# Kernel tuning notes

Measured on AMD Instinct MI355X. Metric: run time of the kernel, lower is better.

## Reference

```python
import jax, jax.numpy as jnp
import numpy as np

EPSILON = 0.1      # init kwarg epsilon
NUM_STAB = 1e-06   # init kwarg num_stab
B, D, C = 4096, 3072, 10


def setup_inputs() -> dict:
    key = jax.random.key(0)
    k1, k2 = jax.random.split(key)
    data = jax.random.normal(k1, (B, D), dtype=jnp.float32)
    # small scale keeps softmax probs near-uniform -> rho well-conditioned
    W = jax.random.normal(k2, (D, C), dtype=jnp.float32) * 0.02
    return {"data": data, "W": W}


def _probs(logits, c):
    # output = softmax(...) * (1 - c*num_stab) + num_stab  (numerical stabilization)
    p = jax.nn.softmax(logits, axis=-1)
    return p * (1.0 - c * NUM_STAB) + NUM_STAB


def reference(data, W):
    c = W.shape[1]
    m = c - 1

    def g(x):  # x: [D] -> new_output row: [m]
        p = _probs(x @ W, c)
        s = jnp.sqrt(p)
        return 2.0 * s[:m] / (1.0 - s[m])

    # Vectorized Jacobian: replaces the m sequential autograd.grad calls.
    jac = jax.vmap(jax.jacrev(g))(data)            # [B, m, D]

    p = _probs(data @ W, c)                        # [B, C]
    s_m = jnp.sqrt(p[:, m])                        # [B]
    delta = 2.0 * jnp.arccos(jnp.sqrt(p / c).sum(axis=1))   # [B]
    rho = (2.0 * (1.0 - s_m) - p[:, :m].sum(axis=1)) / (1.0 - s_m)  # [B]
    jac_norm = jnp.sqrt(jnp.square(jac).sum(axis=(1, 2)))   # [B] Frobenius norm per sample
    reg = jax.nn.elu(jac_norm - delta / (rho * EPSILON))
    return reg.mean()
```

## Files before the change

kernel.cpp:

```cpp
#include <hip/hip_runtime.h>
#include <math.h>

#define NB 4096
#define ND 3072
#define NC 10
#define NM 9

static constexpr float kEps     = 0.1f;
static constexpr float kNumStab = 1e-6f;
static constexpr float kAlpha   = 1.0f - (float)NC * kNumStab;
static constexpr float kInvSqrtC = 0.31622776601683794f;

__global__ void gram_kernel(const float* __restrict__ W, float* __restrict__ G) {
    const int j = blockIdx.x / NC;
    const int k = blockIdx.x % NC;
    float acc = 0.0f;
    for (int d = threadIdx.x; d < ND; d += 256) {
        acc += W[d * NC + j] * W[d * NC + k];
    }
    #pragma unroll
    for (int off = 32; off > 0; off >>= 1) acc += __shfl_xor(acc, off, 64);
    __shared__ float part[4];
    const int lane = threadIdx.x & 63;
    const int wv   = threadIdx.x >> 6;
    if (lane == 0) part[wv] = acc;
    __syncthreads();
    if (threadIdx.x == 0) G[blockIdx.x] = part[0] + part[1] + part[2] + part[3];
}

__global__ __launch_bounds__(256) void jacreg_kernel(
        const float* __restrict__ data, const float* __restrict__ W,
        const float* __restrict__ G, float* __restrict__ out) {
    __shared__ float Gs[100];
    __shared__ float zpart[4][40];
    __shared__ float zsum[40];
    __shared__ float regs[4];

    const int tid  = threadIdx.x;
    const int lane = tid & 63;
    const int wv   = tid >> 6;
    if (tid < 100) Gs[tid] = G[tid];

    const int s0 = blockIdx.x * 4;

    float acc[4][10];
    #pragma unroll
    for (int s = 0; s < 4; ++s)
        #pragma unroll
        for (int k = 0; k < NC; ++k) acc[s][k] = 0.0f;

    const int dwave = wv * 768;
    #pragma unroll
    for (int it = 0; it < 3; ++it) {
        const int d0 = dwave + it * 256 + lane * 4;
        float4 xv[4];
        #pragma unroll
        for (int s = 0; s < 4; ++s) {
            xv[s] = *reinterpret_cast<const float4*>(
                        &data[(size_t)(s0 + s) * ND + d0]);
        }
        #pragma unroll
        for (int dd = 0; dd < 4; ++dd) {
            const float* wr = &W[(size_t)(d0 + dd) * NC];
            const float2 w01 = *reinterpret_cast<const float2*>(wr);
            const float2 w23 = *reinterpret_cast<const float2*>(wr + 2);
            const float2 w45 = *reinterpret_cast<const float2*>(wr + 4);
            const float2 w67 = *reinterpret_cast<const float2*>(wr + 6);
            const float2 w89 = *reinterpret_cast<const float2*>(wr + 8);
            const float wk[10] = {w01.x, w01.y, w23.x, w23.y, w45.x,
                                  w45.y, w67.x, w67.y, w89.x, w89.y};
            #pragma unroll
            for (int s = 0; s < 4; ++s) {
                const float xs[4] = {xv[s].x, xv[s].y, xv[s].z, xv[s].w};
                const float xd = xs[dd];
                #pragma unroll
                for (int k = 0; k < NC; ++k)
                    acc[s][k] = fmaf(xd, wk[k], acc[s][k]);
            }
        }
    }

    #pragma unroll
    for (int s = 0; s < 4; ++s) {
        #pragma unroll
        for (int k = 0; k < NC; ++k) {
            float v = acc[s][k];
            #pragma unroll
            for (int off = 32; off > 0; off >>= 1) v += __shfl_xor(v, off, 64);
            acc[s][k] = v;
        }
    }

    if (lane < 40) {
        float v = 0.0f;
        #pragma unroll
        for (int s = 0; s < 4; ++s)
            #pragma unroll
            for (int k = 0; k < NC; ++k)
                if (lane == s * NC + k) v = acc[s][k];
        zpart[wv][lane] = v;
    }
    __syncthreads();
    if (tid < 40)
        zsum[tid] = zpart[0][tid] + zpart[1][tid] + zpart[2][tid] + zpart[3][tid];
    __syncthreads();

    if (tid < 4) {
        float z[NC];
        #pragma unroll
        for (int k = 0; k < NC; ++k) z[k] = zsum[tid * NC + k];

        float zm = z[0];
        #pragma unroll
        for (int k = 1; k < NC; ++k) zm = fmaxf(zm, z[k]);
        float e[NC], Zs = 0.0f;
        #pragma unroll
        for (int k = 0; k < NC; ++k) { e[k] = expf(z[k] - zm); Zs += e[k]; }
        const float inv = 1.0f / Zs;

        float sg[NC], p[NC], sq[NC], u[NC];
        #pragma unroll
        for (int k = 0; k < NC; ++k) {
            sg[k] = e[k] * inv;
            p[k]  = kAlpha * sg[k] + kNumStab;
            sq[k] = sqrtf(p[k]);
            u[k]  = sg[k] / sq[k];
        }
        const float q = 1.0f - sq[NM];

        float v[NC], t = 0.0f;
        #pragma unroll
        for (int k = 0; k < NC; ++k) {
            float a = 0.0f;
            #pragma unroll
            for (int j = 0; j < NC; ++j) a = fmaf(Gs[k * NC + j], sg[j], a);
            v[k] = a;
            t = fmaf(sg[k], a, t);
        }
        const float vM = v[NM], uM = u[NM];
        const float QMM = Gs[NC * NC - 1] - 2.0f * vM + t;

        float sumJ = 0.0f;
        #pragma unroll
        for (int i = 0; i < NM; ++i) {
            const float Qii = Gs[i * NC + i] - 2.0f * v[i] + t;
            const float QiM = Gs[i * NC + NM] - v[i] - vM + t;
            const float r = sq[i] / q;
            sumJ += u[i] * u[i] * Qii
                  + 2.0f * u[i] * uM * r * QiM
                  + uM * uM * r * r * QMM;
        }
        const float jn = (kAlpha / q) * sqrtf(fmaxf(sumJ, 0.0f));

        float ssum = 0.0f;
        #pragma unroll
        for (int k = 0; k < NC; ++k) ssum += sq[k];
        const float ac = fminf(1.0f, fmaxf(-1.0f, ssum * kInvSqrtC));
        const float delta = 2.0f * acosf(ac);

        float psum = 0.0f;
        #pragma unroll
        for (int k = 0; k < NM; ++k) psum += p[k];
        const float rho = (2.0f * q - psum) / q;

        const float a = jn - delta / (rho * kEps);
        regs[tid] = (a > 0.0f) ? a : expm1f(a);
    }
    __syncthreads();
    if (tid == 0) {
        const float bs = (regs[0] + regs[1] + regs[2] + regs[3]) * (1.0f / (float)NB);
        atomicAdd(out, bs);
    }
}

extern "C" void kernel_launch(void* const* d_in, const int* in_sizes, int n_in,
                              void* d_out, int out_size, void* d_ws, size_t ws_size,
                              hipStream_t stream) {
    const float* data = (const float*)d_in[0];
    const float* W    = (const float*)d_in[1];
    float* out = (float*)d_out;
    float* G   = (float*)d_ws;

    hipMemsetAsync(out, 0, sizeof(float), stream);
    gram_kernel<<<NC * NC, 256, 0, stream>>>(W, G);
    jacreg_kernel<<<NB / 4, 256, 0, stream>>>(data, W, G, out);
}
```

Before: 112.8 us.

## Stage transposed W in LDS and assign two samples per wavefront

Each block now copies W into shared memory in transposed [C][D] layout (120 KB), then each wavefront handles two full sample rows over all of D with a software-prefetched float4 loop, reading W as float4 from LDS. This removes the cross-wave shared-memory reduction and repeated global reads of W from every block. The cost is a 120 KB LDS fill per block, which limits occupancy to one block per CU, and a strided transposed write pattern that may cause bank conflicts. Only 256 blocks are launched, so CU coverage becomes coarse.

```diff
diff --git a/kernel.cpp b/kernel.cpp
--- a/kernel.cpp
+++ b/kernel.cpp
@@ -6,9 +6,9 @@
 #define NC 10
 #define NM 9
 
-static constexpr float kEps     = 0.1f;
-static constexpr float kNumStab = 1e-6f;
-static constexpr float kAlpha   = 1.0f - (float)NC * kNumStab;
+static constexpr float kEps      = 0.1f;
+static constexpr float kNumStab  = 1e-6f;
+static constexpr float kAlpha    = 1.0f - (float)NC * kNumStab;
 static constexpr float kInvSqrtC = 0.31622776601683794f;
 
 __global__ void gram_kernel(const float* __restrict__ W, float* __restrict__ G) {
@@ -28,60 +28,67 @@
     if (threadIdx.x == 0) G[blockIdx.x] = part[0] + part[1] + part[2] + part[3];
 }
 
-__global__ __launch_bounds__(256) void jacreg_kernel(
+__global__ __launch_bounds__(512) void jacreg_kernel(
         const float* __restrict__ data, const float* __restrict__ W,
         const float* __restrict__ G, float* __restrict__ out) {
+    __shared__ float Wts[NC * ND];
     __shared__ float Gs[100];
-    __shared__ float zpart[4][40];
-    __shared__ float zsum[40];
-    __shared__ float regs[4];
+    __shared__ float regs[16];
 
     const int tid  = threadIdx.x;
     const int lane = tid & 63;
     const int wv   = tid >> 6;
+
     if (tid < 100) Gs[tid] = G[tid];
 
-    const int s0 = blockIdx.x * 4;
+    for (int i = tid; i < (ND * NC) / 4; i += 512) {
+        const float4 w4 = reinterpret_cast<const float4*>(W)[i];
+        const float* wp = reinterpret_cast<const float*>(&w4);
+        const int e0 = i * 4;
+        #pragma unroll
+        for (int j = 0; j < 4; ++j) {
+            const int e = e0 + j;
+            Wts[(e % NC) * ND + (e / NC)] = wp[j];
+        }
+    }
+    __syncthreads();
 
-    float acc[4][10];
+    const int s0 = blockIdx.x * 16 + wv * 2;
+    const float* __restrict__ r0 = data + (size_t)s0 * ND;
+    const float* __restrict__ r1 = r0 + ND;
+
+    float acc[2][NC];
     #pragma unroll
-    for (int s = 0; s < 4; ++s)
+    for (int s = 0; s < 2; ++s)
         #pragma unroll
         for (int k = 0; k < NC; ++k) acc[s][k] = 0.0f;
 
-    const int dwave = wv * 768;
-    #pragma unroll
-    for (int it = 0; it < 3; ++it) {
-        const int d0 = dwave + it * 256 + lane * 4;
-        float4 xv[4];
+    float4 x0 = reinterpret_cast<const float4*>(r0)[lane];
+    float4 x1 = reinterpret_cast<const float4*>(r1)[lane];
+    for (int it = 0; it < 12; ++it) {
+        const int nit = (it == 11) ? 11 : it + 1;
+        const float4 nx0 = reinterpret_cast<const float4*>(r0)[nit * 64 + lane];
+        const float4 nx1 = reinterpret_cast<const float4*>(r1)[nit * 64 + lane];
+
+        const int dbase = it * 256 + lane * 4;
         #pragma unroll
-        for (int s = 0; s < 4; ++s) {
-            xv[s] = *reinterpret_cast<const float4*>(
-                        &data[(size_t)(s0 + s) * ND + d0]);
+        for (int k = 0; k < NC; ++k) {
+            const float4 wt = *reinterpret_cast<const float4*>(&Wts[k * ND + dbase]);
+            acc[0][k] = fmaf(x0.x, wt.x, acc[0][k]);
+            acc[0][k] = fmaf(x0.y, wt.y, acc[0][k]);
+            acc[0][k] = fmaf(x0.z, wt.z, acc[0][k]);
+            acc[0][k] = fmaf(x0.w, wt.w, acc[0][k]);
+            acc[1][k] = fmaf(x1.x, wt.x, acc[1][k]);
+            acc[1][k] = fmaf(x1.y, wt.y, acc[1][k]);
+            acc[1][k] = fmaf(x1.z, wt.z, acc[1][k]);
+            acc[1][k] = fmaf(x1.w, wt.w, acc[1][k]);
         }
-        #pragma unroll
-        for (int dd = 0; dd < 4; ++dd) {
-            const float* wr = &W[(size_t)(d0 + dd) * NC];
-            const float2 w01 = *reinterpret_cast<const float2*>(wr);
-            const float2 w23 = *reinterpret_cast<const float2*>(wr + 2);
-            const float2 w45 = *reinterpret_cast<const float2*>(wr + 4);
-            const float2 w67 = *reinterpret_cast<const float2*>(wr + 6);
-            const float2 w89 = *reinterpret_cast<const float2*>(wr + 8);
-            const float wk[10] = {w01.x, w01.y, w23.x, w23.y, w45.x,
-                                  w45.y, w67.x, w67.y, w89.x, w89.y};
-            #pragma unroll
-            for (int s = 0; s < 4; ++s) {
-                const float xs[4] = {xv[s].x, xv[s].y, xv[s].z, xv[s].w};
-                const float xd = xs[dd];
-                #pragma unroll
-                for (int k = 0; k < NC; ++k)
-                    acc[s][k] = fmaf(xd, wk[k], acc[s][k]);
-            }
-        }
+        x0 = nx0;
+        x1 = nx1;
     }
 
     #pragma unroll
-    for (int s = 0; s < 4; ++s) {
+    for (int s = 0; s < 2; ++s)
         #pragma unroll
         for (int k = 0; k < NC; ++k) {
             float v = acc[s][k];
@@ -89,26 +96,11 @@
             for (int off = 32; off > 0; off >>= 1) v += __shfl_xor(v, off, 64);
             acc[s][k] = v;
         }
-    }
 
-    if (lane < 40) {
-        float v = 0.0f;
-        #pragma unroll
-        for (int s = 0; s < 4; ++s)
-            #pragma unroll
-            for (int k = 0; k < NC; ++k)
-                if (lane == s * NC + k) v = acc[s][k];
-        zpart[wv][lane] = v;
-    }
-    __syncthreads();
-    if (tid < 40)
-        zsum[tid] = zpart[0][tid] + zpart[1][tid] + zpart[2][tid] + zpart[3][tid];
-    __syncthreads();
-
-    if (tid < 4) {
+    if (lane < 2) {
         float z[NC];
         #pragma unroll
-        for (int k = 0; k < NC; ++k) z[k] = zsum[tid * NC + k];
+        for (int k = 0; k < NC; ++k) z[k] = (lane == 0) ? acc[0][k] : acc[1][k];
 
         float zm = z[0];
         #pragma unroll
@@ -164,12 +156,14 @@
         const float rho = (2.0f * q - psum) / q;
 
         const float a = jn - delta / (rho * kEps);
-        regs[tid] = (a > 0.0f) ? a : expm1f(a);
+        regs[wv * 2 + lane] = (a > 0.0f) ? a : expm1f(a);
     }
     __syncthreads();
     if (tid == 0) {
-        const float bs = (regs[0] + regs[1] + regs[2] + regs[3]) * (1.0f / (float)NB);
-        atomicAdd(out, bs);
+        float bs = 0.0f;
+        #pragma unroll
+        for (int i = 0; i < 16; ++i) bs += regs[i];
+        atomicAdd(out, bs * (1.0f / (float)NB));
     }
 }
 
@@ -183,5 +177,5 @@
 
     hipMemsetAsync(out, 0, sizeof(float), stream);
     gram_kernel<<<NC * NC, 256, 0, stream>>>(W, G);
-    jacreg_kernel<<<NB / 4, 256, 0, stream>>>(data, W, G, out);
+    jacreg_kernel<<<NB / 16, 512, 0, stream>>>(data, W, G, out);
 }
```

Result: faster. 98.51 us (-12.6%).
